# Optimization experiments

Hardware: AMD Instinct MI355X
Metric: run time of the kernel (lower is better)

The kernel has to match this reference:

```python
import jax, jax.numpy as jnp
import numpy as np

N = 50000   # nodes
E = 600000  # edges
D = 128     # hidden dim
L = 3       # layers

def _gelu(x):
    return jax.nn.gelu(x, approximate=False)  # torch nn.GELU default (erf)

def setup_inputs() -> dict:
    key = jax.random.key(0)
    ks = jax.random.split(key, 20)
    s = 0.05
    return {
        "feats": jax.random.normal(ks[0], (N, D), dtype=jnp.float32),
        "edge_src": jax.random.randint(ks[1], (E,), 0, N),
        "edge_dst": jax.random.randint(ks[2], (E,), 0, N),
        "Win": jax.random.normal(ks[3], (D, D), dtype=jnp.float32) * s,
        "bin_": jnp.zeros((D,), dtype=jnp.float32),
        "Wk": jax.random.normal(ks[4], (L, D, D), dtype=jnp.float32) * s,
        "bk": jnp.zeros((L, D), dtype=jnp.float32),
        "Wq": jax.random.normal(ks[5], (L, D, D), dtype=jnp.float32) * s,
        "bq": jnp.zeros((L, D), dtype=jnp.float32),
        "Wv": jax.random.normal(ks[6], (L, D, D), dtype=jnp.float32) * s,
        "bv": jnp.zeros((L, D), dtype=jnp.float32),
        "Wl": jax.random.normal(ks[7], (L, D, D), dtype=jnp.float32) * s,
        "bl": jnp.zeros((L, D), dtype=jnp.float32),
        "Wout": jax.random.normal(ks[8], (D, 1), dtype=jnp.float32) * s,
        "bout": jnp.zeros((1,), dtype=jnp.float32),
    }

def reference(feats, edge_src, edge_dst, Win, bin_, Wk, bk, Wq, bq, Wv, bv, Wl, bl, Wout, bout):
    # input linear -> (dropout=identity) -> GELU
    h = _gelu(feats @ Win + bin_)
    # in-degree for mean aggregation (clamp to 1 to avoid div by zero)
    deg = jax.ops.segment_sum(jnp.ones((E,), h.dtype), edge_dst, num_segments=N)
    deg = jnp.maximum(deg, 1.0)[:, None]  # [N,1]
    for i in range(L):
        resid = h
        # norm='none' -> identity
        key_n = h @ Wk[i] + bk[i]    # [N,D] source transform
        qry_n = h @ Wq[i] + bq[i]    # [N,D] destination transform
        # SIRConv: per-edge message act(key[src] + query[dst]), mean over incoming edges
        msg = _gelu(key_n[edge_src] + qry_n[edge_dst])          # [E,D]
        agg = jax.ops.segment_sum(msg, edge_dst, num_segments=N) / deg  # [N,D]
        conv = agg @ Wv[i] + bv[i]
        # (dropout=identity) -> GELU -> linear -> (dropout=identity) -> residual
        h = _gelu(conv) @ Wl[i] + bl[i]
        h = h + resid
    # output norm='none' -> output linear -> squeeze(1)
    out = h @ Wout + bout  # [N,1]
    return jnp.squeeze(out, axis=1)
```

## Files before the change

kernel.cpp:

```cpp
#include <hip/hip_runtime.h>
#include <hip/hip_bf16.h>
#include <math.h>

#define NN 50000
#define EE 600000
#define DIM 128
#define LL 3
#define SCB 256
#define NBLK ((NN + SCB - 1) / SCB)
#define CTS 132

typedef float f32x16 __attribute__((ext_vector_type(16)));
typedef short bfrag __attribute__((ext_vector_type(8)));

__device__ __forceinline__ float gelu_f(float x) {
    return 0.5f * x * (1.0f + erff(x * 0.70710678118654752440f));
}

__device__ __forceinline__ ushort f2bf(float x) {
    union { float f; uint u; } v; v.f = x;
    uint r = v.u + 0x7fffu + ((v.u >> 16) & 1u);
    return (ushort)(r >> 16);
}
__device__ __forceinline__ float bf2f(ushort h) {
    union { uint u; float f; } v; v.u = ((uint)h) << 16;
    return v.f;
}

__global__ __launch_bounds__(256) void deg_kernel(const int* __restrict__ dst,
                                                  int* __restrict__ deg) {
    int e = blockIdx.x * blockDim.x + threadIdx.x;
    if (e < EE) atomicAdd(&deg[dst[e]], 1);
}

__global__ __launch_bounds__(256)
void partial_kernel(const int* __restrict__ deg, int* __restrict__ partial) {
    __shared__ int s[256];
    const int t = threadIdx.x;
    const int n = blockIdx.x * SCB + t;
    s[t] = (n < NN) ? deg[n] : 0;
    __syncthreads();
#pragma unroll
    for (int off = 128; off > 0; off >>= 1) {
        if (t < off) s[t] += s[t + off];
        __syncthreads();
    }
    if (t == 0) partial[blockIdx.x] = s[0];
}

__global__ __launch_bounds__(256)
void scanpart_kernel(const int* __restrict__ partial, int* __restrict__ pofs) {
    __shared__ int s[256];
    const int t = threadIdx.x;
    const int own = (t < NBLK) ? partial[t] : 0;
    s[t] = own;
    __syncthreads();
#pragma unroll
    for (int off = 1; off < 256; off <<= 1) {
        int v = s[t];
        int a = (t >= off) ? s[t - off] : 0;
        __syncthreads();
        s[t] = v + a;
        __syncthreads();
    }
    if (t < NBLK) pofs[t] = s[t] - own;
}

__global__ __launch_bounds__(256)
void fill_kernel(const int* __restrict__ deg, const int* __restrict__ pofs,
                 int* __restrict__ rowptr, int* __restrict__ cursor,
                 float* __restrict__ invdeg) {
    __shared__ int s[256];
    const int t = threadIdx.x;
    const int n = blockIdx.x * SCB + t;
    const int d = (n < NN) ? deg[n] : 0;
    s[t] = d;
    __syncthreads();
#pragma unroll
    for (int off = 1; off < 256; off <<= 1) {
        int v = s[t];
        int a = (t >= off) ? s[t - off] : 0;
        __syncthreads();
        s[t] = v + a;
        __syncthreads();
    }
    const int base = pofs[blockIdx.x] + s[t] - d;
    if (n < NN) {
        rowptr[n] = base;
        cursor[n] = base;
        invdeg[n] = 1.0f / (float)(d < 1 ? 1 : d);
        if (n == NN - 1) rowptr[NN] = base + d;
    }
}

__global__ __launch_bounds__(256)
void bucket_kernel(const int* __restrict__ src, const int* __restrict__ dst,
                   int* __restrict__ cursor, int* __restrict__ ebuf) {
    int e = blockIdx.x * blockDim.x + threadIdx.x;
    if (e < EE) {
        int slot = atomicAdd(&cursor[dst[e]], 1);
        ebuf[slot] = src[e];
    }
}

__global__ __launch_bounds__(256)
void wsplit_kernel(const float* __restrict__ Win, const float* __restrict__ Wk,
                   const float* __restrict__ Wq, const float* __restrict__ Wv,
                   const float* __restrict__ Wl, ushort* __restrict__ pre) {
    const int b = blockIdx.x;
    const int m = b >> 1, c = b & 1;
    const float* W;
    if (m == 0) W = Win;
    else if (m <= 3) W = Wk + (size_t)(m - 1) * DIM * DIM;
    else if (m <= 6) W = Wq + (size_t)(m - 4) * DIM * DIM;
    else if (m <= 9) W = Wv + (size_t)(m - 7) * DIM * DIM;
    else W = Wl + (size_t)(m - 10) * DIM * DIM;
    ushort* dst = pre + (size_t)m * (4 * 1024 * 8) + (size_t)c * (2 * 1024 * 8);

    const int t = threadIdx.x;
    const int kc0 = c * 64;
    const int n = t & 127, kh = t >> 7;
    const int cf = n >> 5;
#pragma unroll
    for (int g = 0; g < 4; ++g) {
        const int kl0 = kh * 32 + g * 8;
#pragma unroll
        for (int j = 0; j < 8; ++j) {
            float x = W[(size_t)(kc0 + kl0 + j) * DIM + n];
            ushort hb = f2bf(x);
            float r = x - bf2f(hb);
            const int ks = kl0 >> 4, half = (kl0 >> 3) & 1;
            const int slot = (ks * 4 + cf) * 64 + (n & 31) + 32 * half;
            dst[slot * 8 + j] = hb;
            dst[1024 * 8 + slot * 8 + j] = f2bf(r);
        }
    }
}

__global__ __launch_bounds__(256)
void agg_kernel(const float* __restrict__ key, const float* qry,
                const int* __restrict__ rowptr, const int* __restrict__ ebuf,
                const float* __restrict__ invdeg, float* agg) {
    int tid = blockIdx.x * blockDim.x + threadIdx.x;
    int n = tid >> 6;
    if (n >= NN) return;
    int c = (tid & 63) << 1;
    const float2 q2 = *(const float2*)(qry + (size_t)n * DIM + c);
    float ax = 0.f, ay = 0.f;
    int j = rowptr[n];
    const int hi = rowptr[n + 1];
    for (; j + 8 <= hi; j += 8) {
        float2 k[8];
#pragma unroll
        for (int u = 0; u < 8; ++u)
            k[u] = *(const float2*)(key + (size_t)ebuf[j + u] * DIM + c);
#pragma unroll
        for (int u = 0; u < 8; ++u) {
            ax += gelu_f(k[u].x + q2.x);
            ay += gelu_f(k[u].y + q2.y);
        }
    }
    for (; j < hi; ++j) {
        const float2 k2 = *(const float2*)(key + (size_t)ebuf[j] * DIM + c);
        ax += gelu_f(k2.x + q2.x);
        ay += gelu_f(k2.y + q2.y);
    }
    const float inv = invdeg[n];
    *(float2*)(agg + (size_t)n * DIM + c) = make_float2(ax * inv, ay * inv);
}

enum { EPI_NONE = 0, EPI_GELU = 1, EPI_RESID = 2 };

__device__ __forceinline__ void stage_A(const float* __restrict__ A, int M,
                                        int row0, int kc0, int t,
                                        ushort* Ah, ushort* Al) {
    const int row = t >> 2, ks = t & 3;
    const int grow = row0 + row;
    float f[16];
    if (grow < M) {
        const float* p = A + (size_t)grow * DIM + kc0 + ks * 16;
        float4 q0 = *(const float4*)(p + 0);
        float4 q1 = *(const float4*)(p + 4);
        float4 q2 = *(const float4*)(p + 8);
        float4 q3 = *(const float4*)(p + 12);
        f[0]=q0.x; f[1]=q0.y; f[2]=q0.z; f[3]=q0.w;
        f[4]=q1.x; f[5]=q1.y; f[6]=q1.z; f[7]=q1.w;
        f[8]=q2.x; f[9]=q2.y; f[10]=q2.z; f[11]=q2.w;
        f[12]=q3.x; f[13]=q3.y; f[14]=q3.z; f[15]=q3.w;
    } else {
#pragma unroll
        for (int i = 0; i < 16; ++i) f[i] = 0.f;
    }
#pragma unroll
    for (int h = 0; h < 2; ++h) {
        bfrag hv, lv;
#pragma unroll
        for (int j = 0; j < 8; ++j) {
            float x = f[h * 8 + j];
            ushort hb = f2bf(x);
            float r = x - bf2f(hb);
            hv[j] = (short)hb;
            lv[j] = (short)f2bf(r);
        }
        const int slot = (ks * 2 + (row >> 5)) * 64 + (row & 31) + 32 * h;
        *(bfrag*)&Ah[slot * 8] = hv;
        *(bfrag*)&Al[slot * 8] = lv;
    }
}

template <int EPI>
__device__ __forceinline__ void epilogue(float* Ct, const f32x16& acc0,
                                         const f32x16& acc1, int t, int rblk,
                                         int ch, int l, int row0,
                                         const float* __restrict__ bias,
                                         const float* __restrict__ resid,
                                         float* __restrict__ C, int M) {
    __syncthreads();
    {
        const int colbase = ch * 64 + (l & 31);
        const int rb = rblk * 32 + 4 * (l >> 5);
#pragma unroll
        for (int cf2 = 0; cf2 < 2; ++cf2) {
            const int col = colbase + cf2 * 32;
#pragma unroll
            for (int r = 0; r < 16; ++r) {
                const int rl = rb + (r & 3) + 8 * (r >> 2);
                Ct[rl * CTS + col] = (cf2 == 0 ? acc0[r] : acc1[r]);
            }
        }
    }
    __syncthreads();
    {
        const int rl = t >> 2, j = t & 3;
        const int grow = row0 + rl;
        if (grow < M) {
            float* cp = C + (size_t)grow * DIM;
            const float* rp = (EPI == EPI_RESID) ? resid + (size_t)grow * DIM : nullptr;
#pragma unroll
            for (int i = 0; i < 8; ++i) {
                const int c0 = (j + 4 * i) * 4;
                float4 v = *(const float4*)&Ct[rl * CTS + c0];
                const float4 b4 = *(const float4*)&bias[c0];
                v.x += b4.x; v.y += b4.y; v.z += b4.z; v.w += b4.w;
                if (EPI == EPI_GELU) {
                    v.x = gelu_f(v.x); v.y = gelu_f(v.y);
                    v.z = gelu_f(v.z); v.w = gelu_f(v.w);
                }
                if (EPI == EPI_RESID) {
                    const float4 r4 = *(const float4*)&rp[c0];
                    v.x += r4.x; v.y += r4.y; v.z += r4.z; v.w += r4.w;
                }
                *(float4*)&cp[c0] = v;
            }
        }
    }
    __syncthreads();
}

template <int EPI>
__global__ __launch_bounds__(256)
void gemm_mfma(const float* __restrict__ A, const ushort* __restrict__ wpre,
               const float* __restrict__ bias, const float* __restrict__ resid,
               float* __restrict__ C, int M) {
    __shared__ char smem[49152];
    ushort* Ah = (ushort*)smem;
    ushort* Al = (ushort*)(smem + 8192);
    ushort* Wh = (ushort*)(smem + 16384);
    ushort* Wl = (ushort*)(smem + 32768);
    float* Ct = (float*)smem;

    const int t = threadIdx.x;
    const int row0 = blockIdx.x * 64;
    const int w = t >> 6, l = t & 63;
    const int rblk = w & 1, ch = w >> 1;

    f32x16 acc0, acc1;
#pragma unroll
    for (int i = 0; i < 16; ++i) { acc0[i] = 0.f; acc1[i] = 0.f; }

    for (int c = 0; c < 2; ++c) {
        stage_A(A, M, row0, c * 64, t, Ah, Al);
        {
            const float4* gh = (const float4*)(wpre + ((size_t)c * 2 + 0) * 1024 * 8);
            const float4* gl = (const float4*)(wpre + ((size_t)c * 2 + 1) * 1024 * 8);
            float4* sh = (float4*)Wh;
            float4* sl = (float4*)Wl;
#pragma unroll
            for (int i = 0; i < 4; ++i) {
                sh[i * 256 + t] = gh[i * 256 + t];
                sl[i * 256 + t] = gl[i * 256 + t];
            }
        }
        __syncthreads();
#pragma unroll
        for (int ks = 0; ks < 4; ++ks) {
            const bfrag ah = *(const bfrag*)&Ah[((ks * 2 + rblk) * 64 + l) * 8];
            const bfrag al = *(const bfrag*)&Al[((ks * 2 + rblk) * 64 + l) * 8];
#pragma unroll
            for (int q = 0; q < 2; ++q) {
                const int cf = ch * 2 + q;
                const bfrag bh = *(const bfrag*)&Wh[((ks * 4 + cf) * 64 + l) * 8];
                const bfrag bl = *(const bfrag*)&Wl[((ks * 4 + cf) * 64 + l) * 8];
                f32x16& acc = q == 0 ? acc0 : acc1;
                acc = __builtin_amdgcn_mfma_f32_32x32x16_bf16(al, bh, acc, 0, 0, 0);
                acc = __builtin_amdgcn_mfma_f32_32x32x16_bf16(ah, bl, acc, 0, 0, 0);
                acc = __builtin_amdgcn_mfma_f32_32x32x16_bf16(ah, bh, acc, 0, 0, 0);
            }
        }
        __syncthreads();
    }
    epilogue<EPI>(Ct, acc0, acc1, t, rblk, ch, l, row0, bias, resid, C, M);
}

__global__ __launch_bounds__(256)
void gemm_mfma_kq(const float* __restrict__ A, const ushort* __restrict__ wkpre,
                  const ushort* __restrict__ wqpre, const float* __restrict__ bkb,
                  const float* __restrict__ bqb, float* __restrict__ K,
                  float* __restrict__ Q, int M) {
    __shared__ char smem[81920];
    ushort* Ah  = (ushort*)smem;
    ushort* Al  = (ushort*)(smem + 8192);
    ushort* Wkh = (ushort*)(smem + 16384);
    ushort* Wkl = (ushort*)(smem + 32768);
    ushort* Wqh = (ushort*)(smem + 49152);
    ushort* Wql = (ushort*)(smem + 65536);
    float* Ct = (float*)smem;

    const int t = threadIdx.x;
    const int row0 = blockIdx.x * 64;
    const int w = t >> 6, l = t & 63;
    const int rblk = w & 1, ch = w >> 1;

    f32x16 ak0, ak1, aq0, aq1;
#pragma unroll
    for (int i = 0; i < 16; ++i) { ak0[i] = 0.f; ak1[i] = 0.f; aq0[i] = 0.f; aq1[i] = 0.f; }

    for (int c = 0; c < 2; ++c) {
        stage_A(A, M, row0, c * 64, t, Ah, Al);
        {
            const float4* gkh = (const float4*)(wkpre + ((size_t)c * 2 + 0) * 1024 * 8);
            const float4* gkl = (const float4*)(wkpre + ((size_t)c * 2 + 1) * 1024 * 8);
            const float4* gqh = (const float4*)(wqpre + ((size_t)c * 2 + 0) * 1024 * 8);
            const float4* gql = (const float4*)(wqpre + ((size_t)c * 2 + 1) * 1024 * 8);
            float4* skh = (float4*)Wkh;
            float4* skl = (float4*)Wkl;
            float4* sqh = (float4*)Wqh;
            float4* sql = (float4*)Wql;
#pragma unroll
            for (int i = 0; i < 4; ++i) {
                skh[i * 256 + t] = gkh[i * 256 + t];
                skl[i * 256 + t] = gkl[i * 256 + t];
                sqh[i * 256 + t] = gqh[i * 256 + t];
                sql[i * 256 + t] = gql[i * 256 + t];
            }
        }
        __syncthreads();
#pragma unroll
        for (int ks = 0; ks < 4; ++ks) {
            const bfrag ah = *(const bfrag*)&Ah[((ks * 2 + rblk) * 64 + l) * 8];
            const bfrag al = *(const bfrag*)&Al[((ks * 2 + rblk) * 64 + l) * 8];
#pragma unroll
            for (int q = 0; q < 2; ++q) {
                const int cf = ch * 2 + q;
                const int so = ((ks * 4 + cf) * 64 + l) * 8;
                {
                    const bfrag bh = *(const bfrag*)&Wkh[so];
                    const bfrag bl = *(const bfrag*)&Wkl[so];
                    f32x16& acc = q == 0 ? ak0 : ak1;
                    acc = __builtin_amdgcn_mfma_f32_32x32x16_bf16(al, bh, acc, 0, 0, 0);
                    acc = __builtin_amdgcn_mfma_f32_32x32x16_bf16(ah, bl, acc, 0, 0, 0);
                    acc = __builtin_amdgcn_mfma_f32_32x32x16_bf16(ah, bh, acc, 0, 0, 0);
                }
                {
                    const bfrag bh = *(const bfrag*)&Wqh[so];
                    const bfrag bl = *(const bfrag*)&Wql[so];
                    f32x16& acc = q == 0 ? aq0 : aq1;
                    acc = __builtin_amdgcn_mfma_f32_32x32x16_bf16(al, bh, acc, 0, 0, 0);
                    acc = __builtin_amdgcn_mfma_f32_32x32x16_bf16(ah, bl, acc, 0, 0, 0);
                    acc = __builtin_amdgcn_mfma_f32_32x32x16_bf16(ah, bh, acc, 0, 0, 0);
                }
            }
        }
        __syncthreads();
    }
    epilogue<EPI_NONE>(Ct, ak0, ak1, t, rblk, ch, l, row0, bkb, nullptr, K, M);
    epilogue<EPI_NONE>(Ct, aq0, aq1, t, rblk, ch, l, row0, bqb, nullptr, Q, M);
}

__global__ __launch_bounds__(256)
void out_kernel(const float* __restrict__ h, const float* __restrict__ Wout,
                const float* __restrict__ bout, float* __restrict__ out) {
    int tid = blockIdx.x * blockDim.x + threadIdx.x;
    int n = tid >> 5;
    if (n >= NN) return;
    int lane = tid & 31;
    const float4 h4 = *(const float4*)(h + (size_t)n * DIM + lane * 4);
    const float4 w4 = *(const float4*)(Wout + lane * 4);
    float s = h4.x * w4.x + h4.y * w4.y + h4.z * w4.z + h4.w * w4.w;
#pragma unroll
    for (int off = 16; off > 0; off >>= 1) s += __shfl_down(s, off, 32);
    if (lane == 0) out[n] = s + bout[0];
}

extern "C" void kernel_launch(void* const* d_in, const int* in_sizes, int n_in,
                              void* d_out, int out_size, void* d_ws, size_t ws_size,
                              hipStream_t stream) {
    const float* feats = (const float*)d_in[0];
    const int* esrc = (const int*)d_in[1];
    const int* edst = (const int*)d_in[2];
    const float* Win = (const float*)d_in[3];
    const float* bin_ = (const float*)d_in[4];
    const float* Wk = (const float*)d_in[5];
    const float* bk = (const float*)d_in[6];
    const float* Wq = (const float*)d_in[7];
    const float* bq = (const float*)d_in[8];
    const float* Wv = (const float*)d_in[9];
    const float* bv = (const float*)d_in[10];
    const float* Wl = (const float*)d_in[11];
    const float* bl = (const float*)d_in[12];
    const float* Wout = (const float*)d_in[13];
    const float* bout = (const float*)d_in[14];

    float* ws = (float*)d_ws;
    const size_t ND = (size_t)NN * DIM;
    float* h0 = ws;
    float* h1 = ws + ND;
    float* key = ws + 2 * ND;
    float* qry = ws + 3 * ND;
    float* invdeg = ws + 4 * ND;
    int* deg = (int*)(ws + 4 * ND + NN);
    int* rowptr = deg + NN;
    int* cursor = rowptr + NN + 1;
    int* ebuf = cursor + NN;
    int* partial = ebuf + EE;
    int* pofs = partial + NBLK;
    size_t intofs = (size_t)((pofs + NBLK) - (int*)d_ws);
    intofs = (intofs + 3) & ~(size_t)3;
    ushort* pre = (ushort*)((int*)d_ws + intofs);

    dim3 b256(256);
    const int GB = (NN + 63) / 64;
    const size_t WPM = 4 * 1024 * 8;

    wsplit_kernel<<<26, b256, 0, stream>>>(Win, Wk, Wq, Wv, Wl, pre);

    hipMemsetAsync(deg, 0, NN * sizeof(int), stream);
    deg_kernel<<<(EE + 255) / 256, b256, 0, stream>>>(edst, deg);
    partial_kernel<<<NBLK, b256, 0, stream>>>(deg, partial);
    scanpart_kernel<<<1, b256, 0, stream>>>(partial, pofs);
    fill_kernel<<<NBLK, b256, 0, stream>>>(deg, pofs, rowptr, cursor, invdeg);
    bucket_kernel<<<(EE + 255) / 256, b256, 0, stream>>>(esrc, edst, cursor, ebuf);

    gemm_mfma<EPI_GELU><<<GB, b256, 0, stream>>>(feats, pre, bin_, nullptr, h0, NN);

    const float* hin = h0;
    float* hout = h1;
    for (int i = 0; i < LL; ++i) {
        const ushort* wk = pre + (size_t)(1 + i) * WPM;
        const ushort* wq = pre + (size_t)(4 + i) * WPM;
        const ushort* wv = pre + (size_t)(7 + i) * WPM;
        const ushort* wl = pre + (size_t)(10 + i) * WPM;
        const float* bki = bk + (size_t)i * DIM;
        const float* bqi = bq + (size_t)i * DIM;
        const float* bvi = bv + (size_t)i * DIM;
        const float* bli = bl + (size_t)i * DIM;

        gemm_mfma_kq<<<GB, b256, 0, stream>>>(hin, wk, wq, bki, bqi, key, qry, NN);
        agg_kernel<<<(NN * 64) / 256, b256, 0, stream>>>(key, qry, rowptr, ebuf,
                                                         invdeg, qry);
        gemm_mfma<EPI_GELU><<<GB, b256, 0, stream>>>(qry, wv, bvi, nullptr, key, NN);
        gemm_mfma<EPI_RESID><<<GB, b256, 0, stream>>>(key, wl, bli, hin, hout, NN);
        float* tmp = (float*)hin;
        hin = hout;
        hout = tmp;
    }
    out_kernel<<<(NN * 32 + 255) / 256, b256, 0, stream>>>(hin, Wout, bout,
                                                           (float*)d_out);
}
```

Baseline: 537.1 us.

## Fuse Wv and Wl GEMMs into one kernel keeping intermediate in registers

Merges the GELU(agg@Wv+bv) GEMM and the following @Wl+residual GEMM into one kernel. The intermediate tile is written to shared memory, split into bf16 hi/lo fragments held in registers, and used as the A operand of the second GEMM. This removes one kernel launch and a full N×D fp32 write and read of the intermediate per layer, at the cost of more registers per thread. The agg kernel's gather unroll also drops from 8 to 4, which lowers register pressure but leaves fewer loads in flight.

After: 501.7 us. 1.07x faster.

```diff
diff --git a/kernel.cpp b/kernel.cpp
--- a/kernel.cpp
+++ b/kernel.cpp
@@ -149,19 +149,20 @@
     float ax = 0.f, ay = 0.f;
     int j = rowptr[n];
     const int hi = rowptr[n + 1];
-    for (; j + 8 <= hi; j += 8) {
-        float2 k[8];
-#pragma unroll
-        for (int u = 0; u < 8; ++u)
-            k[u] = *(const float2*)(key + (size_t)ebuf[j + u] * DIM + c);
-#pragma unroll
-        for (int u = 0; u < 8; ++u) {
-            ax += gelu_f(k[u].x + q2.x);
-            ay += gelu_f(k[u].y + q2.y);
-        }
+    for (; j + 4 <= hi; j += 4) {
+        const int s0 = ebuf[j], s1 = ebuf[j + 1], s2 = ebuf[j + 2], s3 = ebuf[j + 3];
+        const float2 k0 = *(const float2*)(key + (size_t)s0 * DIM + c);
+        const float2 k1 = *(const float2*)(key + (size_t)s1 * DIM + c);
+        const float2 k2 = *(const float2*)(key + (size_t)s2 * DIM + c);
+        const float2 k3 = *(const float2*)(key + (size_t)s3 * DIM + c);
+        ax += gelu_f(k0.x + q2.x); ay += gelu_f(k0.y + q2.y);
+        ax += gelu_f(k1.x + q2.x); ay += gelu_f(k1.y + q2.y);
+        ax += gelu_f(k2.x + q2.x); ay += gelu_f(k2.y + q2.y);
+        ax += gelu_f(k3.x + q2.x); ay += gelu_f(k3.y + q2.y);
     }
     for (; j < hi; ++j) {
-        const float2 k2 = *(const float2*)(key + (size_t)ebuf[j] * DIM + c);
+        const int s = ebuf[j];
+        const float2 k2 = *(const float2*)(key + (size_t)s * DIM + c);
         ax += gelu_f(k2.x + q2.x);
         ay += gelu_f(k2.y + q2.y);
     }
@@ -208,6 +209,19 @@
     }
 }
 
+__device__ __forceinline__ void stage_W(const ushort* __restrict__ wpre, int c,
+                                        int t, ushort* Wh, ushort* Wl) {
+    const float4* gh = (const float4*)(wpre + ((size_t)c * 2 + 0) * 1024 * 8);
+    const float4* gl = (const float4*)(wpre + ((size_t)c * 2 + 1) * 1024 * 8);
+    float4* sh = (float4*)Wh;
+    float4* sl = (float4*)Wl;
+#pragma unroll
+    for (int i = 0; i < 4; ++i) {
+        sh[i * 256 + t] = gh[i * 256 + t];
+        sl[i * 256 + t] = gl[i * 256 + t];
+    }
+}
+
 template <int EPI>
 __device__ __forceinline__ void epilogue(float* Ct, const f32x16& acc0,
                                          const f32x16& acc1, int t, int rblk,
@@ -280,17 +294,7 @@
 
     for (int c = 0; c < 2; ++c) {
         stage_A(A, M, row0, c * 64, t, Ah, Al);
-        {
-            const float4* gh = (const float4*)(wpre + ((size_t)c * 2 + 0) * 1024 * 8);
-            const float4* gl = (const float4*)(wpre + ((size_t)c * 2 + 1) * 1024 * 8);
-            float4* sh = (float4*)Wh;
-            float4* sl = (float4*)Wl;
-#pragma unroll
-            for (int i = 0; i < 4; ++i) {
-                sh[i * 256 + t] = gh[i * 256 + t];
-                sl[i * 256 + t] = gl[i * 256 + t];
-            }
-        }
+        stage_W(wpre, c, t, Wh, Wl);
         __syncthreads();
 #pragma unroll
         for (int ks = 0; ks < 4; ++ks) {
@@ -337,23 +341,8 @@
 
     for (int c = 0; c < 2; ++c) {
         stage_A(A, M, row0, c * 64, t, Ah, Al);
-        {
-            const float4* gkh = (const float4*)(wkpre + ((size_t)c * 2 + 0) * 1024 * 8);
-            const float4* gkl = (const float4*)(wkpre + ((size_t)c * 2 + 1) * 1024 * 8);
-            const float4* gqh = (const float4*)(wqpre + ((size_t)c * 2 + 0) * 1024 * 8);
-            const float4* gql = (const float4*)(wqpre + ((size_t)c * 2 + 1) * 1024 * 8);
-            float4* skh = (float4*)Wkh;
-            float4* skl = (float4*)Wkl;
-            float4* sqh = (float4*)Wqh;
-            float4* sql = (float4*)Wql;
-#pragma unroll
-            for (int i = 0; i < 4; ++i) {
-                skh[i * 256 + t] = gkh[i * 256 + t];
-                skl[i * 256 + t] = gkl[i * 256 + t];
-                sqh[i * 256 + t] = gqh[i * 256 + t];
-                sql[i * 256 + t] = gql[i * 256 + t];
-            }
-        }
+        stage_W(wkpre, c, t, Wkh, Wkl);
+        stage_W(wqpre, c, t, Wqh, Wql);
         __syncthreads();
 #pragma unroll
         for (int ks = 0; ks < 4; ++ks) {
@@ -388,6 +377,112 @@
 }
 
 __global__ __launch_bounds__(256)
+void gemm_mfma_vl(const float* __restrict__ A, const ushort* __restrict__ wvpre,
+                  const ushort* __restrict__ wlpre, const float* __restrict__ bvb,
+                  const float* __restrict__ blb, const float* __restrict__ resid,
+                  float* __restrict__ C, int M) {
+    __shared__ char smem[49152];
+    ushort* Ah = (ushort*)smem;
+    ushort* Al = (ushort*)(smem + 8192);
+    ushort* Wh = (ushort*)(smem + 16384);
+    ushort* Wl = (ushort*)(smem + 32768);
+    float* Ct = (float*)smem;
+
+    const int t = threadIdx.x;
+    const int row0 = blockIdx.x * 64;
+    const int w = t >> 6, l = t & 63;
+    const int rblk = w & 1, ch = w >> 1;
+
+    f32x16 acc0, acc1;
+#pragma unroll
+    for (int i = 0; i < 16; ++i) { acc0[i] = 0.f; acc1[i] = 0.f; }
+
+    for (int c = 0; c < 2; ++c) {
+        stage_A(A, M, row0, c * 64, t, Ah, Al);
+        stage_W(wvpre, c, t, Wh, Wl);
+        __syncthreads();
+#pragma unroll
+        for (int ks = 0; ks < 4; ++ks) {
+            const bfrag ah = *(const bfrag*)&Ah[((ks * 2 + rblk) * 64 + l) * 8];
+            const bfrag al = *(const bfrag*)&Al[((ks * 2 + rblk) * 64 + l) * 8];
+#pragma unroll
+            for (int q = 0; q < 2; ++q) {
+                const int cf = ch * 2 + q;
+                const bfrag bh = *(const bfrag*)&Wh[((ks * 4 + cf) * 64 + l) * 8];
+                const bfrag bl = *(const bfrag*)&Wl[((ks * 4 + cf) * 64 + l) * 8];
+                f32x16& acc = q == 0 ? acc0 : acc1;
+                acc = __builtin_amdgcn_mfma_f32_32x32x16_bf16(al, bh, acc, 0, 0, 0);
+                acc = __builtin_amdgcn_mfma_f32_32x32x16_bf16(ah, bl, acc, 0, 0, 0);
+                acc = __builtin_amdgcn_mfma_f32_32x32x16_bf16(ah, bh, acc, 0, 0, 0);
+            }
+        }
+        __syncthreads();
+    }
+    {
+        const int colbase = ch * 64 + (l & 31);
+        const int rb = rblk * 32 + 4 * (l >> 5);
+#pragma unroll
+        for (int cf2 = 0; cf2 < 2; ++cf2) {
+            const int col = colbase + cf2 * 32;
+            const float bv = bvb[col];
+#pragma unroll
+            for (int r = 0; r < 16; ++r) {
+                const int rl = rb + (r & 3) + 8 * (r >> 2);
+                Ct[rl * CTS + col] = gelu_f((cf2 == 0 ? acc0[r] : acc1[r]) + bv);
+            }
+        }
+    }
+    __syncthreads();
+    bfrag tah[2][4], tal[2][4];
+    {
+        const int trow = rblk * 32 + (l & 31);
+        const int khalf = (l >> 5) * 8;
+#pragma unroll
+        for (int c = 0; c < 2; ++c)
+#pragma unroll
+            for (int ks = 0; ks < 4; ++ks) {
+                const float* p = &Ct[trow * CTS + c * 64 + ks * 16 + khalf];
+                bfrag hv, lv;
+#pragma unroll
+                for (int j = 0; j < 8; ++j) {
+                    float x = p[j];
+                    ushort hb = f2bf(x);
+                    float r = x - bf2f(hb);
+                    hv[j] = (short)hb;
+                    lv[j] = (short)f2bf(r);
+                }
+                tah[c][ks] = hv;
+                tal[c][ks] = lv;
+            }
+    }
+    __syncthreads();
+    f32x16 bcc0, bcc1;
+#pragma unroll
+    for (int i = 0; i < 16; ++i) { bcc0[i] = 0.f; bcc1[i] = 0.f; }
+    for (int c = 0; c < 2; ++c) {
+        stage_W(wlpre, c, t, Wh, Wl);
+        __syncthreads();
+#pragma unroll
+        for (int ks = 0; ks < 4; ++ks) {
+            const bfrag ah = tah[c][ks];
+            const bfrag al = tal[c][ks];
+#pragma unroll
+            for (int q = 0; q < 2; ++q) {
+                const int cf = ch * 2 + q;
+                const bfrag bh = *(const bfrag*)&Wh[((ks * 4 + cf) * 64 + l) * 8];
+                const bfrag bl = *(const bfrag*)&Wl[((ks * 4 + cf) * 64 + l) * 8];
+                f32x16& acc = q == 0 ? bcc0 : bcc1;
+                acc = __builtin_amdgcn_mfma_f32_32x32x16_bf16(al, bh, acc, 0, 0, 0);
+                acc = __builtin_amdgcn_mfma_f32_32x32x16_bf16(ah, bl, acc, 0, 0, 0);
+                acc = __builtin_amdgcn_mfma_f32_32x32x16_bf16(ah, bh, acc, 0, 0, 0);
+            }
+        }
+        __syncthreads();
+    }
+    epilogue<EPI_RESID>(Ct, bcc0, bcc1, t, rblk, ch, l, row0, blb, resid, C, M);
+}
+
+__global__ __launch_bounds__(256)
 void out_kernel(const float* __restrict__ h, const float* __restrict__ Wout,
                 const float* __restrict__ bout, float* __restrict__ out) {
     int tid = blockIdx.x * blockDim.x + threadIdx.x;
@@ -468,8 +563,7 @@
         gemm_mfma_kq<<<GB, b256, 0, stream>>>(hin, wk, wq, bki, bqi, key, qry, NN);
         agg_kernel<<<(NN * 64) / 256, b256, 0, stream>>>(key, qry, rowptr, ebuf,
                                                          invdeg, qry);
-        gemm_mfma<EPI_GELU><<<GB, b256, 0, stream>>>(qry, wv, bvi, nullptr, key, NN);
-        gemm_mfma<EPI_RESID><<<GB, b256, 0, stream>>>(key, wl, bli, hin, hout, NN);
+        gemm_mfma_vl<<<GB, b256, 0, stream>>>(qry, wv, wl, bvi, bli, hin, hout, NN);
         float* tmp = (float*)hin;
         hin = hout;
         hout = tmp;
```
